# Kernel tuning notes

Hardware: AMD Instinct MI355X
Metric: run time of the kernel (lower is better)

## Reference

```python
import jax, jax.numpy as jnp
import numpy as np
from functools import partial

B, T, I, H, S = 256, 512, 128, 256, 4  # batch, seq_len, input_size, hidden_size, num_segments


def setup_inputs() -> dict:
    key = jax.random.key(0)
    ks = jax.random.split(key, 6)
    x = jax.random.normal(ks[0], (B, T, I), dtype=jnp.float32)
    # variable-length sequences so segment indexing floor(t*S/len) is exercised
    lengths = jax.random.randint(ks[1], (B,), T // 2, T + 1)
    mask = jnp.arange(T)[None, :] < lengths[:, None]  # [B, T] bool
    s = 1.0 / np.sqrt(H)  # torch LSTMCell init: U(-1/sqrt(H), 1/sqrt(H))
    W_ih = jax.random.uniform(ks[2], (S, 4 * H, I), minval=-s, maxval=s, dtype=jnp.float32)
    W_hh = jax.random.uniform(ks[3], (S, 4 * H, H), minval=-s, maxval=s, dtype=jnp.float32)
    b_ih = jax.random.uniform(ks[4], (S, 4 * H), minval=-s, maxval=s, dtype=jnp.float32)
    b_hh = jax.random.uniform(ks[5], (S, 4 * H), minval=-s, maxval=s, dtype=jnp.float32)
    return {"x": x, "mask": mask, "W_ih": W_ih, "W_hh": W_hh, "b_ih": b_ih, "b_hh": b_hh}


def _shift_lstm(x, mask, W_ih, W_hh, b_ih, b_hh):
    # dropout is identity in eval mode
    Bb, Tt, _ = x.shape
    lengths = jnp.maximum(mask.astype(jnp.int32).sum(-1), 1)  # clamp_min(1)
    t = jnp.arange(Tt)
    seg = jnp.minimum((t[None, :] * S) // lengths[:, None], S - 1)  # [B, T]
    bias = (b_ih + b_hh)[None]  # [1, S, 4H]

    def step(carry, inputs):
        h, c = carry
        x_t, seg_t, valid = inputs  # [B,I], [B], [B]
        # gates for every segment cell, then pick each sample's segment
        gates = (jnp.einsum('bi,soi->bso', x_t, W_ih)
                 + jnp.einsum('bh,soh->bso', h, W_hh) + bias)  # [B, S, 4H]
        g = jnp.take_along_axis(gates, seg_t[:, None, None], axis=1)[:, 0, :]  # [B, 4H]
        i_g, f_g, g_g, o_g = jnp.split(g, 4, axis=-1)  # torch LSTMCell gate order i,f,g,o
        c_new = jax.nn.sigmoid(f_g) * c + jax.nn.sigmoid(i_g) * jnp.tanh(g_g)
        h_new = jax.nn.sigmoid(o_g) * jnp.tanh(c_new)
        v = valid[:, None]
        h = jnp.where(v, h_new, h)
        c = jnp.where(v, c_new, c)
        out = jnp.where(v, h, jnp.zeros_like(h))  # padded steps stay zero
        return (h, c), out

    h0 = jnp.zeros((Bb, H), dtype=x.dtype)
    c0 = jnp.zeros((Bb, H), dtype=x.dtype)
    xs = (x.transpose(1, 0, 2), seg.T, mask.T)
    _, outs = jax.lax.scan(step, (h0, c0), xs)
    outputs = outs.transpose(1, 0, 2)  # [B, T, H]
    last_idx = (lengths - 1)[:, None, None]
    last_outputs = jnp.take_along_axis(outputs, last_idx, axis=1)[:, 0, :]  # [B, H]
    return outputs, last_outputs


def reference(x, mask, W_ih, W_hh, b_ih, b_hh):
    return _shift_lstm(x, mask, W_ih, W_hh, b_ih, b_hh)
```

## Files before the change

kernel.cpp:

```cpp
#include <hip/hip_runtime.h>
#include <math.h>

#define Bb 256
#define Tt 512
#define Ii 128
#define Hh 256
#define Ss 4
#define G4 1024

#define LCH 18
#define VR1 11
#define TILE 8

typedef _Float16 half2t __attribute__((ext_vector_type(2)));
union W16 { uint4 u; half2t h[4]; };
union CV8 { _Float16 h[4]; uint2 u; };

__device__ __forceinline__ float dot8(uint4 w, uint4 hv, float acc) {
  W16 a; a.u = w; W16 b; b.u = hv;
#if __has_builtin(__builtin_amdgcn_fdot2)
  acc = __builtin_amdgcn_fdot2(a.h[0], b.h[0], acc, false);
  acc = __builtin_amdgcn_fdot2(a.h[1], b.h[1], acc, false);
  acc = __builtin_amdgcn_fdot2(a.h[2], b.h[2], acc, false);
  acc = __builtin_amdgcn_fdot2(a.h[3], b.h[3], acc, false);
#else
#pragma unroll
  for (int k = 0; k < 4; k++)
    acc += (float)a.h[k].x * (float)b.h[k].x + (float)a.h[k].y * (float)b.h[k].y;
#endif
  return acc;
}

__global__ void k_len(const int* __restrict__ mask, int* __restrict__ len) {
  int b = blockIdx.x, tid = threadIdx.x;
  int c = (mask[b * Tt + tid] != 0) + (mask[b * Tt + 256 + tid] != 0);
#pragma unroll
  for (int off = 32; off > 0; off >>= 1) c += __shfl_down(c, off, 64);
  __shared__ int red[4];
  if ((tid & 63) == 0) red[tid >> 6] = c;
  __syncthreads();
  if (tid == 0) {
    int t = red[0] + red[1] + red[2] + red[3];
    len[b] = t < 1 ? 1 : t;
  }
}

__global__ void k_tr(const float* __restrict__ W_ih, const float* __restrict__ W_hh,
                     uint4* __restrict__ wt_hh16, uint4* __restrict__ wt_ih16) {
  int id = blockIdx.x * blockDim.x + threadIdx.x;
  const int NH16 = Ss * 32 * G4;
  const int NI16 = Ss * 16 * G4;
  if (id < NH16) {
    int o = id % G4, i8 = (id / G4) % 32, s = id / (G4 * 32);
    const float* src = W_hh + ((size_t)(s * G4 + o)) * Hh + 8 * i8;
    W16 w;
#pragma unroll
    for (int k = 0; k < 4; k++) {
      w.h[k].x = (_Float16)src[2 * k];
      w.h[k].y = (_Float16)src[2 * k + 1];
    }
    wt_hh16[id] = w.u;
  } else if (id < NH16 + NI16) {
    int id3 = id - NH16;
    int o = id3 % G4, i8 = (id3 / G4) % 16, s = id3 / (G4 * 16);
    const float* src = W_ih + ((size_t)(s * G4 + o)) * Ii + 8 * i8;
    W16 w;
#pragma unroll
    for (int k = 0; k < 4; k++) {
      w.h[k].x = (_Float16)src[2 * k];
      w.h[k].y = (_Float16)src[2 * k + 1];
    }
    wt_ih16[id3] = w.u;
  }
}

__global__ __launch_bounds__(512, 2) void k_fused(
    const float* __restrict__ x, const uint4* __restrict__ wt_hh16,
    const uint4* __restrict__ wt_ih16, const float* __restrict__ b_ih,
    const float* __restrict__ b_hh, const int* __restrict__ len,
    float* __restrict__ out) {
  __shared__ __align__(16) uint4 lds_w[LCH * 512];
  __shared__ __align__(16) _Float16 xs[TILE * Ii];
  __shared__ __align__(16) _Float16 h_h[Hh];
  __shared__ float f_sh[Hh];
  __shared__ float o_sh[Hh];
  const int b = blockIdx.x;
  const int tid = threadIdx.x;
  const int u = tid & 255;
  const int pr = tid >> 8;
  const int r0 = u + pr * 256;
  const int r1 = r0 + 512;
  const int L = len[b];
  const int tb1 = (L + 3) >> 2;
  const int tb2 = (2 * L + 3) >> 2;
  const int tb3 = (3 * L + 3) >> 2;
  if (pr == 0) h_h[u] = (_Float16)0.f;
  float c = 0.f;
  float* outb = out + (size_t)b * Tt * Hh;
  float* lastb = out + (size_t)Bb * Tt * Hh + (size_t)b * Hh;
  const uint4* h4 = (const uint4*)h_h;
  const uint4* xs4 = (const uint4*)xs;
  uint4 wh0[32];
  uint4 wr1[VR1];
  int s_cur = -1;
  float xg0[TILE], xg1[TILE];

  for (int t0 = 0; t0 < L; t0 += TILE) {
    if (tid < TILE * Ii / 4) {
      float4 xf = ((const float4*)(x + ((size_t)b * Tt + t0) * Ii))[tid];
      CV8 cv;
      cv.h[0] = (_Float16)xf.x;
      cv.h[1] = (_Float16)xf.y;
      cv.h[2] = (_Float16)xf.z;
      cv.h[3] = (_Float16)xf.w;
      ((uint2*)xs)[tid] = cv.u;
    }
    __syncthreads();

    int segv[TILE];
#pragma unroll
    for (int tt = 0; tt < TILE; tt++) {
      int t = t0 + tt;
      segv[tt] = (t >= tb1) + (t >= tb2) + (t >= tb3);
    }
    const int s_lo = segv[0];
    const int tlast = (t0 + TILE - 1 < L) ? (t0 + TILE - 1) : (L - 1);
    const int s_hi = (tlast >= tb1) + (tlast >= tb2) + (tlast >= tb3);

    for (int s = s_lo; s <= s_hi; s++) {
      float acc0[TILE], acc1[TILE];
#pragma unroll
      for (int tt = 0; tt < TILE; tt++) { acc0[tt] = 0.f; acc1[tt] = 0.f; }
      const uint4* wbi = wt_ih16 + ((size_t)s * 16) * G4;
#pragma unroll 2
      for (int i8 = 0; i8 < 16; i8++) {
        uint4 w0 = wbi[(size_t)i8 * G4 + r0];
        uint4 w1 = wbi[(size_t)i8 * G4 + r1];
#pragma unroll
        for (int tt = 0; tt < TILE; tt++) {
          uint4 hv = xs4[tt * 16 + i8];
          acc0[tt] = dot8(w0, hv, acc0[tt]);
          acc1[tt] = dot8(w1, hv, acc1[tt]);
        }
      }
      float bias0 = b_ih[s * G4 + r0] + b_hh[s * G4 + r0];
      float bias1 = b_ih[s * G4 + r1] + b_hh[s * G4 + r1];
#pragma unroll
      for (int tt = 0; tt < TILE; tt++) {
        if (segv[tt] == s) {
          xg0[tt] = acc0[tt] + bias0;
          xg1[tt] = acc1[tt] + bias1;
        }
      }
    }

#pragma unroll
    for (int tt = 0; tt < TILE; tt++) {
      const int t = t0 + tt;
      if (t < L) {
        const int s = segv[tt];
        if (s != s_cur) {
          s_cur = s;
          const uint4* wb = wt_hh16 + (size_t)s * 32 * G4;
#pragma unroll
          for (int i8 = 0; i8 < 32; i8++) wh0[i8] = wb[(size_t)i8 * G4 + r0];
#pragma unroll
          for (int i8 = 0; i8 < LCH; i8++)
            lds_w[i8 * 512 + tid] = wb[(size_t)i8 * G4 + r1];
#pragma unroll
          for (int k = 0; k < VR1; k++)
            wr1[k] = wb[(size_t)(LCH + k) * G4 + r1];
        }
        const uint4* wbs = wt_hh16 + ((size_t)s_cur * 32) * G4 + r1;
        uint4 st0 = wbs[(size_t)(LCH + VR1 + 0) * G4];
        uint4 st1 = wbs[(size_t)(LCH + VR1 + 1) * G4];
        uint4 st2 = wbs[(size_t)(LCH + VR1 + 2) * G4];
        float a0 = xg0[tt], a1 = xg1[tt];
        float a0b = 0.f, a1b = 0.f;
        __syncthreads();
#pragma unroll
        for (int i8 = 0; i8 < LCH; i8++) {
          uint4 hv = h4[i8];
          uint4 wl = lds_w[i8 * 512 + tid];
          if (i8 & 1) { a0b = dot8(wh0[i8], hv, a0b); a1b = dot8(wl, hv, a1b); }
          else        { a0  = dot8(wh0[i8], hv, a0 ); a1  = dot8(wl, hv, a1 ); }
        }
#pragma unroll
        for (int i8 = LCH; i8 < LCH + VR1; i8++) {
          uint4 hv = h4[i8];
          if (i8 & 1) { a0b = dot8(wh0[i8], hv, a0b); a1b = dot8(wr1[i8 - LCH], hv, a1b); }
          else        { a0  = dot8(wh0[i8], hv, a0 ); a1  = dot8(wr1[i8 - LCH], hv, a1 ); }
        }
        {
          uint4 hv;
          hv = h4[LCH + VR1 + 0];
          a0  = dot8(wh0[LCH + VR1 + 0], hv, a0 );
          a1  = dot8(st0, hv, a1);
          hv = h4[LCH + VR1 + 1];
          a0b = dot8(wh0[LCH + VR1 + 1], hv, a0b);
          a1b = dot8(st1, hv, a1b);
          hv = h4[LCH + VR1 + 2];
          a0  = dot8(wh0[LCH + VR1 + 2], hv, a0 );
          a1  = dot8(st2, hv, a1);
        }
        a0 += a0b;
        a1 += a1b;
        if (pr == 1) {
          f_sh[u] = 1.f / (1.f + expf(-a0));
          o_sh[u] = 1.f / (1.f + expf(-a1));
        }
        __syncthreads();
        if (pr == 0) {
          float ig = 1.f / (1.f + expf(-a0));
          float gg = tanhf(a1);
          c = f_sh[u] * c + ig * gg;
          float h = o_sh[u] * tanhf(c);
          h_h[u] = (_Float16)h;
          outb[(size_t)t * Hh + u] = h;
          if (t == L - 1) lastb[u] = h;
        }
      }
    }
  }
  {
    const int ztotal = (Tt - L) * (Hh / 4);
    float4* zb = (float4*)(outb + (size_t)L * Hh);
    float4 z; z.x = z.y = z.z = z.w = 0.f;
    for (int i = tid; i < ztotal; i += 512) zb[i] = z;
  }
}

extern "C" void kernel_launch(void* const* d_in, const int* in_sizes, int n_in,
                              void* d_out, int out_size, void* d_ws, size_t ws_size,
                              hipStream_t stream) {
  const float* x = (const float*)d_in[0];
  const int* mask = (const int*)d_in[1];
  const float* W_ih = (const float*)d_in[2];
  const float* W_hh = (const float*)d_in[3];
  const float* b_ih = (const float*)d_in[4];
  const float* b_hh = (const float*)d_in[5];
  float* out = (float*)d_out;
  char* ws = (char*)d_ws;

  const size_t HH16_OFF = 0;
  const size_t HH16_BYTES = (size_t)Ss * 32 * G4 * 16;
  const size_t IH16_OFF = HH16_OFF + HH16_BYTES;
  const size_t IH16_BYTES = (size_t)Ss * 16 * G4 * 16;
  const size_t LEN_OFF = IH16_OFF + IH16_BYTES;

  uint4* wt_hh16 = (uint4*)(ws + HH16_OFF);
  uint4* wt_ih16 = (uint4*)(ws + IH16_OFF);
  int* len = (int*)(ws + LEN_OFF);

  k_len<<<Bb, 256, 0, stream>>>(mask, len);
  k_tr<<<768, 256, 0, stream>>>(W_ih, W_hh, wt_hh16, wt_ih16);
  k_fused<<<Bb, 512, 0, stream>>>(x, wt_hh16, wt_ih16, b_ih, b_hh, len, out);
}
```

Baseline: 2.522 ms.

## Rebalance W_hh residency: fewer registers, more LDS, streamed loads interleaved

Changes where the recurrent weights live. Before, the first row's weights sat fully in 32 registers and the second row's were split between LDS and registers, with two blocks per CU. Now 19 chunks go to LDS, only 10 chunks stay in registers, and the remaining 35 chunks are streamed from global/L2 on every timestep, with the loads spread through the dot-product loop so their latency overlaps compute. This lowers register pressure, and the occupancy hint of 2 in launch_bounds is dropped. In exchange, each step now does far more global loads, which adds L2 traffic and latency on the serial recurrence.

```diff
diff --git a/kernel.cpp b/kernel.cpp
--- a/kernel.cpp
+++ b/kernel.cpp
@@ -8,8 +8,6 @@
 #define Ss 4
 #define G4 1024
 
-#define LCH 18
-#define VR1 11
 #define TILE 8
 
 typedef _Float16 half2t __attribute__((ext_vector_type(2)));
@@ -74,12 +72,12 @@
   }
 }
 
-__global__ __launch_bounds__(512, 2) void k_fused(
+__global__ __launch_bounds__(512) void k_fused(
     const float* __restrict__ x, const uint4* __restrict__ wt_hh16,
     const uint4* __restrict__ wt_ih16, const float* __restrict__ b_ih,
     const float* __restrict__ b_hh, const int* __restrict__ len,
     float* __restrict__ out) {
-  __shared__ __align__(16) uint4 lds_w[LCH * 512];
+  __shared__ __align__(16) uint4 lds_w[19 * 512];
   __shared__ __align__(16) _Float16 xs[TILE * Ii];
   __shared__ __align__(16) _Float16 h_h[Hh];
   __shared__ float f_sh[Hh];
@@ -100,8 +98,8 @@
   float* lastb = out + (size_t)Bb * Tt * Hh + (size_t)b * Hh;
   const uint4* h4 = (const uint4*)h_h;
   const uint4* xs4 = (const uint4*)xs;
-  uint4 wh0[32];
-  uint4 wr1[VR1];
+  uint4 w0v[6];
+  uint4 w1v[4];
   int s_cur = -1;
   float xg0[TILE], xg1[TILE];
 
@@ -161,47 +159,51 @@
         const int s = segv[tt];
         if (s != s_cur) {
           s_cur = s;
-          const uint4* wb = wt_hh16 + (size_t)s * 32 * G4;
-#pragma unroll
-          for (int i8 = 0; i8 < 32; i8++) wh0[i8] = wb[(size_t)i8 * G4 + r0];
-#pragma unroll
-          for (int i8 = 0; i8 < LCH; i8++)
-            lds_w[i8 * 512 + tid] = wb[(size_t)i8 * G4 + r1];
-#pragma unroll
-          for (int k = 0; k < VR1; k++)
-            wr1[k] = wb[(size_t)(LCH + k) * G4 + r1];
-        }
-        const uint4* wbs = wt_hh16 + ((size_t)s_cur * 32) * G4 + r1;
-        uint4 st0 = wbs[(size_t)(LCH + VR1 + 0) * G4];
-        uint4 st1 = wbs[(size_t)(LCH + VR1 + 1) * G4];
-        uint4 st2 = wbs[(size_t)(LCH + VR1 + 2) * G4];
+          const uint4* wb0 = wt_hh16 + (size_t)s * 32 * G4 + r0;
+          const uint4* wb1 = wt_hh16 + (size_t)s * 32 * G4 + r1;
+#pragma unroll
+          for (int j = 0; j < 10; j++) lds_w[j * 512 + tid] = wb0[(size_t)j * G4];
+#pragma unroll
+          for (int j = 0; j < 9; j++)
+            lds_w[(10 + j) * 512 + tid] = wb1[(size_t)j * G4];
+#pragma unroll
+          for (int k = 0; k < 6; k++) w0v[k] = wb0[(size_t)(10 + k) * G4];
+#pragma unroll
+          for (int k = 0; k < 4; k++) w1v[k] = wb1[(size_t)(9 + k) * G4];
+        }
+        const uint4* wbs0 = wt_hh16 + (size_t)s_cur * 32 * G4 + r0;
+        const uint4* wbs1 = wt_hh16 + (size_t)s_cur * 32 * G4 + r1;
+        uint4 sA[16], sB[19];
+        sB[0] = wbs1[(size_t)13 * G4];
+        sB[1] = wbs1[(size_t)14 * G4];
+        sB[2] = wbs1[(size_t)15 * G4];
+        sB[3] = wbs1[(size_t)16 * G4];
+        sA[0] = wbs0[(size_t)16 * G4];
+        sA[1] = wbs0[(size_t)17 * G4];
         float a0 = xg0[tt], a1 = xg1[tt];
         float a0b = 0.f, a1b = 0.f;
         __syncthreads();
 #pragma unroll
-        for (int i8 = 0; i8 < LCH; i8++) {
+        for (int i8 = 0; i8 < 32; i8++) {
+          if (i8 == 2) sB[4] = wbs1[(size_t)17 * G4];
+          if (i8 == 5) sB[5] = wbs1[(size_t)18 * G4];
+          if (i8 == 8) sB[6] = wbs1[(size_t)19 * G4];
+          if (i8 == 11) sB[7] = wbs1[(size_t)20 * G4];
+          if (i8 >= 13 && i8 <= 23) {
+            sB[i8 - 5] = wbs1[(size_t)(i8 + 8) * G4];
+            if (i8 >= 14) sA[i8 - 12] = wbs0[(size_t)(i8 + 4) * G4];
+          }
+          if (i8 == 24) sA[12] = wbs0[(size_t)28 * G4];
+          if (i8 == 25) sA[13] = wbs0[(size_t)29 * G4];
+          if (i8 == 26) sA[14] = wbs0[(size_t)30 * G4];
+          if (i8 == 27) sA[15] = wbs0[(size_t)31 * G4];
           uint4 hv = h4[i8];
-          uint4 wl = lds_w[i8 * 512 + tid];
-          if (i8 & 1) { a0b = dot8(wh0[i8], hv, a0b); a1b = dot8(wl, hv, a1b); }
-          else        { a0  = dot8(wh0[i8], hv, a0 ); a1  = dot8(wl, hv, a1 ); }
-        }
-#pragma unroll
-        for (int i8 = LCH; i8 < LCH + VR1; i8++) {
-          uint4 hv = h4[i8];
-          if (i8 & 1) { a0b = dot8(wh0[i8], hv, a0b); a1b = dot8(wr1[i8 - LCH], hv, a1b); }
-          else        { a0  = dot8(wh0[i8], hv, a0 ); a1  = dot8(wr1[i8 - LCH], hv, a1 ); }
-        }
-        {
-          uint4 hv;
-          hv = h4[LCH + VR1 + 0];
-          a0  = dot8(wh0[LCH + VR1 + 0], hv, a0 );
-          a1  = dot8(st0, hv, a1);
-          hv = h4[LCH + VR1 + 1];
-          a0b = dot8(wh0[LCH + VR1 + 1], hv, a0b);
-          a1b = dot8(st1, hv, a1b);
-          hv = h4[LCH + VR1 + 2];
-          a0  = dot8(wh0[LCH + VR1 + 2], hv, a0 );
-          a1  = dot8(st2, hv, a1);
+          uint4 wA = (i8 < 10) ? lds_w[i8 * 512 + tid]
+                   : (i8 < 16) ? w0v[i8 - 10] : sA[i8 - 16];
+          uint4 wB = (i8 < 9) ? lds_w[(10 + i8) * 512 + tid]
+                   : (i8 < 13) ? w1v[i8 - 9] : sB[i8 - 13];
+          if (i8 & 1) { a0b = dot8(wA, hv, a0b); a1b = dot8(wB, hv, a1b); }
+          else        { a0  = dot8(wA, hv, a0 ); a1  = dot8(wB, hv, a1 ); }
         }
         a0 += a0b;
         a1 += a1b;
```

After: 2.143 ms. 1.18x faster.
